# Optimization experiments

Hardware: AMD Instinct MI355X
Metric: run time of the kernel (lower is better)

The kernel has to match this reference:

```python
import jax, jax.numpy as jnp
import numpy as np

PATCH = 16
STRIDE = 8  # patch_size - overlap

def setup_inputs() -> dict:
    key = jax.random.key(0)
    x = jax.random.normal(key, (16, 3, 512, 512), dtype=jnp.float32)
    return {"x": x, "k_neighbors": 8}

def reference(x, k_neighbors):
    B, C, H, W = x.shape
    p, s = PATCH, STRIDE
    nh = (H - p) // s + 1
    nw = (W - p) // s + 1
    N = nh * nw
    # F.unfold equivalent: feature dim ordered (C, kh, kw), then transpose(1,2)
    patches = jax.lax.conv_general_dilated_patches(
        x, filter_shape=(p, p), window_strides=(s, s), padding='VALID')  # [B, C*p*p, nh, nw]
    patches = patches.reshape(B, C * p * p, N).transpose(0, 2, 1)  # [B, N, C*p*p]
    # grid positions [(i, j)] row-major, same order as the python double loop
    ii, jj = jnp.meshgrid(jnp.arange(nh), jnp.arange(nw), indexing='ij')
    pos = jnp.stack([ii.ravel(), jj.ravel()], axis=1).astype(jnp.float32)  # [N, 2]
    positions = jnp.broadcast_to(pos[None], (B, N, 2))
    k = min(int(k_neighbors) + 1, N)
    def knn(posb):
        # squared euclidean distance preserves the ordering of cdist(p=2)
        d2 = jnp.sum((posb[:, None, :] - posb[None, :, :]) ** 2, axis=-1)  # [N, N]
        _, idx = jax.lax.top_k(-d2, k)  # k smallest distances
        tgt = idx[:, 1:]  # drop self (distance 0)
        src = jnp.broadcast_to(jnp.arange(N)[:, None], tgt.shape)
        return jnp.stack([src.ravel(), tgt.ravel()], axis=0)  # [2, N*k_neighbors]
    edge_index = jax.vmap(knn)(positions)  # [B, 2, N*k_neighbors]
    return patches, positions, edge_index
```

## Files before the change

### kernel.cpp

```cpp
#include <hip/hip_runtime.h>

#define BB      16
#define CH      3
#define HH      512
#define WW      512
#define NH      63
#define NW      63
#define NN      3969
#define FDIM    768
#define EDGES   31752

#define PATCHES_ELEMS  (BB * NN * FDIM)
#define POS_ELEMS      (BB * NN * 2)

#define F4        (FDIM / 4)
#define TOTAL_G   (BB * NN * F4)
#define PBLOCKS   3969
#define PTHREADS  (PBLOCKS * 256)
#define ITER      12

#define PE_THREADS (BB * NN)
#define PE_BLOCKS  ((PE_THREADS + 255) / 256)

typedef float  f4 __attribute__((ext_vector_type(4)));
typedef float  f2 __attribute__((ext_vector_type(2)));

__global__ __launch_bounds__(256) void fused_kernel(const float* __restrict__ x,
                                                    float* __restrict__ out) {
    unsigned bid = blockIdx.x;

    if (bid >= PE_BLOCKS) {
        unsigned tid = (bid - PE_BLOCKS) * 256u + threadIdx.x;
#pragma unroll
        for (unsigned k = 0; k < ITER; ++k) {
            unsigned g    = tid + k * PTHREADS;
            unsigned f4i  = g % F4;
            unsigned rest = g / F4;
            unsigned n    = rest % NN;
            unsigned b    = rest / NN;

            unsigned f  = f4i << 2;
            unsigned c  = f >> 8;
            unsigned di = (f >> 4) & 15;
            unsigned dj = f & 15;
            unsigned i  = n / NW;
            unsigned j  = n - i * NW;

            const f4 v = *reinterpret_cast<const f4*>(
                x + ((size_t)((b * CH + c) * HH + i * 8u + di) * WW + j * 8u + dj));
            __builtin_nontemporal_store(v, reinterpret_cast<f4*>(out + (size_t)g * 4));
        }
    } else {
        unsigned g = bid * 256u + threadIdx.x;
        if (g >= PE_THREADS) return;
        unsigned n = g % NN;
        unsigned b = g / NN;
        int i = (int)(n / NW);
        int j = (int)(n - (unsigned)i * NW);

        *reinterpret_cast<f2*>(out + PATCHES_ELEMS + (size_t)(b * NN + n) * 2) =
            f2{(float)i, (float)j};

        unsigned best[9];
#pragma unroll
        for (int s = 0; s < 9; ++s) best[s] = 0xFFFFFFFFu;
        for (int di = -2; di <= 2; ++di) {
            int ni = i + di;
            if (ni < 0 || ni >= NH) continue;
            for (int dj = -2; dj <= 2; ++dj) {
                int nj = j + dj;
                if (nj < 0 || nj >= NW) continue;
                unsigned key = ((unsigned)(di * di + dj * dj) << 12)
                             | (unsigned)(ni * NW + nj);
#pragma unroll
                for (int s = 0; s < 9; ++s) {
                    if (key < best[s]) { unsigned tmp = best[s]; best[s] = key; key = tmp; }
                }
            }
        }

        float src_f = (float)n;
        f4 s4 = {src_f, src_f, src_f, src_f};
        f4 t0 = {(float)(best[1] & 0xFFFu), (float)(best[2] & 0xFFFu),
                 (float)(best[3] & 0xFFFu), (float)(best[4] & 0xFFFu)};
        f4 t1 = {(float)(best[5] & 0xFFFu), (float)(best[6] & 0xFFFu),
                 (float)(best[7] & 0xFFFu), (float)(best[8] & 0xFFFu)};

        float* ebase = out + PATCHES_ELEMS + POS_ELEMS + (size_t)b * 2 * EDGES;
        *reinterpret_cast<f4*>(ebase + (size_t)n * 8)             = s4;
        *reinterpret_cast<f4*>(ebase + (size_t)n * 8 + 4)         = s4;
        *reinterpret_cast<f4*>(ebase + EDGES + (size_t)n * 8)     = t0;
        *reinterpret_cast<f4*>(ebase + EDGES + (size_t)n * 8 + 4) = t1;
    }
}

extern "C" void kernel_launch(void* const* d_in, const int* in_sizes, int n_in,
                              void* d_out, int out_size, void* d_ws, size_t ws_size,
                              hipStream_t stream) {
    const float* x = (const float*)d_in[0];
    float* out     = (float*)d_out;
    fused_kernel<<<PE_BLOCKS + PBLOCKS, 256, 0, stream>>>(x, out);
}
```

Before: 255.4 us.

## Stage input row strips in LDS and emit patches per grid row

Each patch block now loads a 16-row strip of one channel into shared memory, then writes every patch of that grid row from LDS. Previously the overlapping patches were gathered straight from global memory with per-element index divisions. The goal is to remove redundant global reads and the index arithmetic. The cost is fewer blocks, two barriers per channel that serialize load and store phases, and about 33 KB of LDS per block, which may limit occupancy.

```diff
diff --git a/kernel.cpp b/kernel.cpp
--- a/kernel.cpp
+++ b/kernel.cpp
@@ -13,14 +13,11 @@
 #define PATCHES_ELEMS  (BB * NN * FDIM)
 #define POS_ELEMS      (BB * NN * 2)
 
-#define F4        (FDIM / 4)
-#define TOTAL_G   (BB * NN * F4)
-#define PBLOCKS   3969
-#define PTHREADS  (PBLOCKS * 256)
-#define ITER      12
-
 #define PE_THREADS (BB * NN)
 #define PE_BLOCKS  ((PE_THREADS + 255) / 256)
+#define PATCH_BLOCKS (BB * NH)
+
+#define PADW 516
 
 typedef float  f4 __attribute__((ext_vector_type(4)));
 typedef float  f2 __attribute__((ext_vector_type(2)));
@@ -30,25 +27,37 @@
     unsigned bid = blockIdx.x;
 
     if (bid >= PE_BLOCKS) {
-        unsigned tid = (bid - PE_BLOCKS) * 256u + threadIdx.x;
+        unsigned pb = bid - PE_BLOCKS;
+        unsigned b  = pb / NH;
+        unsigned i  = pb % NH;
+        unsigned tid = threadIdx.x;
+
+        __shared__ float lds[16][PADW];
+
+        unsigned lane = tid & 63u;
+        unsigned wave = tid >> 6;
+        unsigned dio  = lane >> 2;
+        unsigned q4   = (lane & 3u) << 2;
+
+        for (unsigned c = 0; c < CH; ++c) {
+            const float* base = x + ((size_t)(b * CH + c) * HH + i * 8u) * WW;
 #pragma unroll
-        for (unsigned k = 0; k < ITER; ++k) {
-            unsigned g    = tid + k * PTHREADS;
-            unsigned f4i  = g % F4;
-            unsigned rest = g / F4;
-            unsigned n    = rest % NN;
-            unsigned b    = rest / NN;
+            for (unsigned u = 0; u < 8; ++u) {
+                unsigned f4id = u * 256u + tid;
+                unsigned di   = f4id >> 7;
+                unsigned col  = (f4id & 127u) << 2;
+                *reinterpret_cast<f4*>(&lds[di][col]) =
+                    *reinterpret_cast<const f4*>(base + (size_t)di * WW + col);
+            }
+            __syncthreads();
 
-            unsigned f  = f4i << 2;
-            unsigned c  = f >> 8;
-            unsigned di = (f >> 4) & 15;
-            unsigned dj = f & 15;
-            unsigned i  = n / NW;
-            unsigned j  = n - i * NW;
-
-            const f4 v = *reinterpret_cast<const f4*>(
-                x + ((size_t)((b * CH + c) * HH + i * 8u + di) * WW + j * 8u + dj));
-            __builtin_nontemporal_store(v, reinterpret_cast<f4*>(out + (size_t)g * 4));
+            for (unsigned j = wave; j < NW; j += 4) {
+                const f4 v = *reinterpret_cast<const f4*>(&lds[dio][j * 8u + q4]);
+                float* dst = out + ((size_t)(b * NN + i * NW + j) * FDIM
+                                    + c * 256u + (lane << 2));
+                __builtin_nontemporal_store(v, reinterpret_cast<f4*>(dst));
+            }
+            __syncthreads();
         }
     } else {
         unsigned g = bid * 256u + threadIdx.x;
@@ -99,5 +108,5 @@
                               hipStream_t stream) {
     const float* x = (const float*)d_in[0];
     float* out     = (float*)d_out;
-    fused_kernel<<<PE_BLOCKS + PBLOCKS, 256, 0, stream>>>(x, out);
+    fused_kernel<<<PE_BLOCKS + PATCH_BLOCKS, 256, 0, stream>>>(x, out);
 }
```

New measurement: 238.9 us. 6.5% less time.
